# Performance work log

Hardware: AMD Instinct MI355X
Metric: run time of the kernel (lower is better)

Reference implementation:

```python
import jax, jax.numpy as jnp
import numpy as np

N_NODES = 50000
N_EDGES = 600000
EMB_DIM = 128
HIDDEN = 128
BN_EPS = 1e-5


def setup_inputs() -> dict:
    key = jax.random.key(0)
    ks = jax.random.split(key, 8)
    s_in = 1.0 / np.sqrt(EMB_DIM)
    s_h = 1.0 / np.sqrt(HIDDEN)
    return {
        "x_idx": jnp.arange(N_NODES, dtype=jnp.int32),
        "edge_index": jax.random.randint(ks[0], (2, N_EDGES), 0, N_NODES, dtype=jnp.int32),
        "emb_table": jax.random.normal(ks[1], (N_NODES, EMB_DIM), jnp.float32),
        # ClusterGCNConv: lin_out (bias=False) and lin_root (bias=False)
        "W_out": jax.random.uniform(ks[2], (HIDDEN, EMB_DIM), jnp.float32, -s_in, s_in),
        "W_root": jax.random.uniform(ks[3], (HIDDEN, EMB_DIM), jnp.float32, -s_in, s_in),
        "bn0_gamma": jnp.ones((HIDDEN,), jnp.float32),
        "bn0_beta": jnp.zeros((HIDDEN,), jnp.float32),
        # SGConv 1 (K=1, add_self_loops=True, Linear with bias)
        "W_sg1": jax.random.uniform(ks[4], (HIDDEN, HIDDEN), jnp.float32, -s_h, s_h),
        "b_sg1": jnp.zeros((HIDDEN,), jnp.float32),
        "bn1_gamma": jnp.ones((HIDDEN,), jnp.float32),
        "bn1_beta": jnp.zeros((HIDDEN,), jnp.float32),
        # SGConv 2 (final layer)
        "W_sg2": jax.random.uniform(ks[5], (HIDDEN, HIDDEN), jnp.float32, -s_h, s_h),
        "b_sg2": jnp.zeros((HIDDEN,), jnp.float32),
    }


def _cluster_gcn(x, row, col, W_out, W_root, n):
    # PyG ClusterGCNConv (add_self_loops=False, diag_lambda=0, bias=False):
    # out[c] = sum_{(r->c)} (1/deg(c)) * x[r];  return out @ W_out^T + x @ W_root^T
    deg = jax.ops.segment_sum(jnp.ones_like(col, dtype=x.dtype), col, num_segments=n)
    deg_inv = 1.0 / jnp.maximum(deg, 1.0)
    msg = x[row] * deg_inv[col][:, None]                  # [E, D]
    agg = jax.ops.segment_sum(msg, col, num_segments=n)   # [N, D]
    return agg @ W_out.T + x @ W_root.T


def _sg_conv(x, row, col, W, b, n):
    # PyG SGConv K=1 with gcn_norm: A_hat = D^{-1/2}(A+I)D^{-1/2}, then Linear.
    loop = jnp.arange(n, dtype=row.dtype)
    r = jnp.concatenate([row, loop])
    c = jnp.concatenate([col, loop])
    deg = jax.ops.segment_sum(jnp.ones_like(c, dtype=x.dtype), c, num_segments=n)
    dis = jnp.where(deg > 0, jax.lax.rsqrt(jnp.maximum(deg, 1e-12)), 0.0)
    ew = dis[r] * dis[c]                                   # [E+N]
    agg = jax.ops.segment_sum(x[r] * ew[:, None], c, num_segments=n)
    return agg @ W.T + b


def _bn(x, gamma, beta):
    # BatchNorm1d in training mode: batch statistics, biased variance.
    mu = x.mean(axis=0)
    var = ((x - mu) ** 2).mean(axis=0)
    return (x - mu) * jax.lax.rsqrt(var + BN_EPS) * gamma + beta


def reference(x_idx, edge_index, emb_table, W_out, W_root, bn0_gamma, bn0_beta,
              W_sg1, b_sg1, bn1_gamma, bn1_beta, W_sg2, b_sg2):
    n = emb_table.shape[0]
    row, col = edge_index[0], edge_index[1]
    x = emb_table[x_idx]                                   # [N, D]
    # layer 0: ClusterGCNConv -> BN -> ReLU (dropout p=0)
    x = _cluster_gcn(x, row, col, W_out, W_root, n)
    x = jax.nn.relu(_bn(x, bn0_gamma, bn0_beta))
    # layer 1: SGConv -> BN -> ReLU
    x = _sg_conv(x, row, col, W_sg1, b_sg1, n)
    x = jax.nn.relu(_bn(x, bn1_gamma, bn1_beta))
    # final SGConv
    return _sg_conv(x, row, col, W_sg2, b_sg2, n)
```

## Files before the change

kernel.cpp:

```cpp
#include <hip/hip_runtime.h>
#include <stdint.h>

#define NN 50000
#define NE 600000
#define DD 128
#define BN_EPS 1e-5f

typedef __attribute__((ext_vector_type(8))) short short8;
typedef __attribute__((ext_vector_type(4))) float f32x4;

__device__ __forceinline__ float bf2f(uint16_t u) {
    union { uint32_t u; float f; } v; v.u = ((uint32_t)u) << 16; return v.f;
}
__device__ __forceinline__ uint16_t f2bf(float f) {
    union { float f; uint32_t u; } v; v.f = f;
    return (uint16_t)((v.u + 0x7FFFu + ((v.u >> 16) & 1u)) >> 16);
}
__device__ __forceinline__ float lo16(uint32_t v) { return bf2f((uint16_t)(v & 0xFFFFu)); }
__device__ __forceinline__ float hi16(uint32_t v) { return bf2f((uint16_t)(v >> 16)); }

__global__ void k_count(const int* __restrict__ col, int* __restrict__ cnt) {
    int e = blockIdx.x * 256 + threadIdx.x;
    if (e < NE) atomicAdd(&cnt[col[e]], 1);
}

__global__ void k_bsum(const int* __restrict__ cnt, int* __restrict__ bsum) {
    __shared__ int s[256];
    int i = blockIdx.x * 256 + threadIdx.x;
    s[threadIdx.x] = (i < NN) ? cnt[i] : 0;
    __syncthreads();
    for (int d = 128; d > 0; d >>= 1) {
        if (threadIdx.x < d) s[threadIdx.x] += s[threadIdx.x + d];
        __syncthreads();
    }
    if (threadIdx.x == 0) bsum[blockIdx.x] = s[0];
}

__global__ void k_bscan(int* __restrict__ bsum, int nb) {
    __shared__ int s[256];
    int t = threadIdx.x;
    int v = (t < nb) ? bsum[t] : 0;
    s[t] = v;
    __syncthreads();
    for (int d = 1; d < 256; d <<= 1) {
        int add = (t >= d) ? s[t - d] : 0;
        __syncthreads();
        s[t] += add;
        __syncthreads();
    }
    if (t < nb) bsum[t] = s[t] - v;
}

__global__ void k_off(const int* __restrict__ cnt, const int* __restrict__ bsum,
                      int* __restrict__ off, float* __restrict__ deginv,
                      float* __restrict__ dis) {
    __shared__ int s[256];
    int t = threadIdx.x;
    int i = blockIdx.x * 256 + t;
    int v = (i < NN) ? cnt[i] : 0;
    s[t] = v;
    __syncthreads();
    for (int d = 1; d < 256; d <<= 1) {
        int add = (t >= d) ? s[t - d] : 0;
        __syncthreads();
        s[t] += add;
        __syncthreads();
    }
    if (i < NN) {
        int excl = s[t] - v + bsum[blockIdx.x];
        off[i] = excl;
        deginv[i] = 1.0f / fmaxf((float)v, 1.0f);
        dis[i] = rsqrtf((float)v + 1.0f);
        if (i == NN - 1) off[NN] = excl + v;
    }
}

__global__ void k_fill(const int* __restrict__ ei, const int* __restrict__ off,
                       int* __restrict__ fill, int* __restrict__ csr_row) {
    int e = blockIdx.x * 256 + threadIdx.x;
    if (e < NE) {
        int c = ei[NE + e];
        int p = atomicAdd(&fill[c], 1);
        csr_row[off[c] + p] = ei[e];
    }
}

__global__ void k_gather(const int* __restrict__ x_idx, const float* __restrict__ emb,
                         uint16_t* __restrict__ xb) {
    int idx = blockIdx.x * 256 + threadIdx.x;
    if (idx >= NN * 32) return;
    int node = idx >> 5, c4 = (idx & 31) << 2;
    int src = x_idx[node];
    float4 v = *(const float4*)(emb + (size_t)src * DD + c4);
    ushort4 o;
    o.x = f2bf(v.x); o.y = f2bf(v.y); o.z = f2bf(v.z); o.w = f2bf(v.w);
    *(ushort4*)(xb + (size_t)node * DD + c4) = o;
}

template<int MODE>
__global__ __launch_bounds__(256)
void k_agg(const uint16_t* __restrict__ xb, const int* __restrict__ off,
           const int* __restrict__ csr_row, const float* __restrict__ deginv,
           const float* __restrict__ dis, uint16_t* __restrict__ aggb) {
    int node = blockIdx.x * 4 + (threadIdx.x >> 6);
    if (node >= NN) return;
    int lane = threadIdx.x & 63;
    const uint32_t* __restrict__ xw = (const uint32_t*)xb;
    float a0 = 0.0f, a1 = 0.0f;
    if (MODE == 1) {
        uint32_t v = xw[(size_t)node * 64 + lane];
        a0 = lo16(v); a1 = hi16(v);
    }
    int s = off[node], e = off[node + 1];
    for (int base = s; base < e; base += 64) {
        int cnt = min(e - base, 64);
        int idxv = (lane < cnt) ? csr_row[base + lane] : 0;
        int i = 0;
        for (; i + 4 <= cnt; i += 4) {
            int r0 = __builtin_amdgcn_readlane(idxv, i);
            int r1 = __builtin_amdgcn_readlane(idxv, i + 1);
            int r2 = __builtin_amdgcn_readlane(idxv, i + 2);
            int r3 = __builtin_amdgcn_readlane(idxv, i + 3);
            uint32_t v0 = xw[(size_t)r0 * 64 + lane];
            uint32_t v1 = xw[(size_t)r1 * 64 + lane];
            uint32_t v2 = xw[(size_t)r2 * 64 + lane];
            uint32_t v3 = xw[(size_t)r3 * 64 + lane];
            a0 += lo16(v0); a1 += hi16(v0);
            a0 += lo16(v1); a1 += hi16(v1);
            a0 += lo16(v2); a1 += hi16(v2);
            a0 += lo16(v3); a1 += hi16(v3);
        }
        for (; i < cnt; ++i) {
            int r = __builtin_amdgcn_readlane(idxv, i);
            uint32_t v = xw[(size_t)r * 64 + lane];
            a0 += lo16(v); a1 += hi16(v);
        }
    }
    float sc = (MODE == 1) ? dis[node] : deginv[node];
    a0 *= sc; a1 *= sc;
    uint32_t o = (uint32_t)f2bf(a0) | ((uint32_t)f2bf(a1) << 16);
    *(uint32_t*)(aggb + (size_t)node * DD + lane * 2) = o;
}

template<bool DUAL, bool STATS, bool BIAS>
__global__ __launch_bounds__(256, 2)
void k_gemm(const uint16_t* __restrict__ A1, const uint16_t* __restrict__ A2,
            const float* __restrict__ W1, const float* __restrict__ W2,
            const float* __restrict__ bias, float* __restrict__ H,
            float* __restrict__ stats) {
    __shared__ uint16_t Alds[128 * 128];
    __shared__ uint16_t Wlds[128 * 128];
    const int t = threadIdx.x;
    const int lane = t & 63, wid = t >> 6;
    const int wm = (wid >> 1) * 64, wn = (wid & 1) * 64;
    const int m0 = blockIdx.x * 128;
    f32x4 zero = {0.0f, 0.0f, 0.0f, 0.0f};
    f32x4 acc[4][4];
    #pragma unroll
    for (int m = 0; m < 4; ++m)
        #pragma unroll
        for (int n = 0; n < 4; ++n) acc[m][n] = zero;

    const int NP = DUAL ? 2 : 1;
    for (int p = 0; p < NP; ++p) {
        const uint16_t* A = (DUAL && p) ? A2 : A1;
        const float* W = (DUAL && p) ? W2 : W1;
        if (p) __syncthreads();
        #pragma unroll
        for (int it = 0; it < 8; ++it) {
            int idx = it * 256 + t;
            int row = idx >> 4, c16 = idx & 15;
            uint32_t boff = (uint32_t)(row * 256 + ((c16 * 16) ^ ((row & 7) << 4)));
            uint4 v = make_uint4(0u, 0u, 0u, 0u);
            if (m0 + row < NN)
                v = *(const uint4*)(A + (size_t)(m0 + row) * DD + c16 * 8);
            *(uint4*)((char*)Alds + boff) = v;
        }
        #pragma unroll
        for (int it = 0; it < 8; ++it) {
            int idx = it * 256 + t;
            int row = idx >> 4, c8 = idx & 15;
            const float* wp = W + row * DD + c8 * 8;
            float4 v0 = *(const float4*)(wp);
            float4 v1 = *(const float4*)(wp + 4);
            uint4 pk;
            pk.x = (uint32_t)f2bf(v0.x) | ((uint32_t)f2bf(v0.y) << 16);
            pk.y = (uint32_t)f2bf(v0.z) | ((uint32_t)f2bf(v0.w) << 16);
            pk.z = (uint32_t)f2bf(v1.x) | ((uint32_t)f2bf(v1.y) << 16);
            pk.w = (uint32_t)f2bf(v1.z) | ((uint32_t)f2bf(v1.w) << 16);
            uint32_t boff = (uint32_t)(row * 256 + ((c8 * 16) ^ ((row & 7) << 4)));
            *(uint4*)((char*)Wlds + boff) = pk;
        }
        __syncthreads();
        #pragma unroll
        for (int ks = 0; ks < 4; ++ks) {
            short8 a[4], b[4];
            int kb = ks * 64 + ((lane >> 4) << 4);
            #pragma unroll
            for (int m = 0; m < 4; ++m) {
                int row = wm + m * 16 + (lane & 15);
                a[m] = *(const short8*)((const char*)Alds + row * 256 + (kb ^ ((row & 7) << 4)));
            }
            #pragma unroll
            for (int n = 0; n < 4; ++n) {
                int row = wn + n * 16 + (lane & 15);
                b[n] = *(const short8*)((const char*)Wlds + row * 256 + (kb ^ ((row & 7) << 4)));
            }
            #pragma unroll
            for (int m = 0; m < 4; ++m)
                #pragma unroll
                for (int n = 0; n < 4; ++n)
                    acc[m][n] = __builtin_amdgcn_mfma_f32_16x16x32_bf16(a[m], b[n], acc[m][n], 0, 0, 0);
        }
    }
    #pragma unroll
    for (int n = 0; n < 4; ++n) {
        int col = wn + n * 16 + (lane & 15);
        float bb = BIAS ? bias[col] : 0.0f;
        float ssum = 0.0f, ssq = 0.0f;
        #pragma unroll
        for (int m = 0; m < 4; ++m) {
            int rbase = m0 + wm + m * 16 + ((lane >> 4) << 2);
            #pragma unroll
            for (int i = 0; i < 4; ++i) {
                int gr = rbase + i;
                if (gr < NN) {
                    float v = acc[m][n][i] + bb;
                    H[(size_t)gr * DD + col] = v;
                    ssum += v; ssq += v * v;
                }
            }
        }
        if (STATS) {
            ssum += __shfl_xor(ssum, 16, 64);
            ssum += __shfl_xor(ssum, 32, 64);
            ssq  += __shfl_xor(ssq, 16, 64);
            ssq  += __shfl_xor(ssq, 32, 64);
            if (lane < 16) {
                atomicAdd(&stats[col], ssum);
                atomicAdd(&stats[DD + col], ssq);
            }
        }
    }
}

__global__ void k_bnprep(float* __restrict__ st, const float* __restrict__ gamma,
                         const float* __restrict__ beta) {
    int c = threadIdx.x;
    if (c < DD) {
        const float invn = 1.0f / (float)NN;
        float mean = st[c] * invn;
        float var = st[DD + c] * invn - mean * mean;
        float sc = gamma[c] * rsqrtf(var + BN_EPS);
        st[256 + c] = sc;
        st[384 + c] = beta[c] - mean * sc;
    }
}

__global__ void k_bnrelu(const float* __restrict__ H, const float* __restrict__ st,
                         const float* __restrict__ dis, uint16_t* __restrict__ xb) {
    int idx = blockIdx.x * 256 + threadIdx.x;
    if (idx >= NN * 32) return;
    int node = idx >> 5, c4 = (idx & 31) << 2;
    float d = dis[node];
    float4 v = *(const float4*)(H + (size_t)node * DD + c4);
    float r0 = fmaxf(v.x * st[256 + c4 + 0] + st[384 + c4 + 0], 0.0f) * d;
    float r1 = fmaxf(v.y * st[256 + c4 + 1] + st[384 + c4 + 1], 0.0f) * d;
    float r2 = fmaxf(v.z * st[256 + c4 + 2] + st[384 + c4 + 2], 0.0f) * d;
    float r3 = fmaxf(v.w * st[256 + c4 + 3] + st[384 + c4 + 3], 0.0f) * d;
    ushort4 o;
    o.x = f2bf(r0); o.y = f2bf(r1); o.z = f2bf(r2); o.w = f2bf(r3);
    *(ushort4*)(xb + (size_t)node * DD + c4) = o;
}

extern "C" void kernel_launch(void* const* d_in, const int* in_sizes, int n_in,
                              void* d_out, int out_size, void* d_ws, size_t ws_size,
                              hipStream_t stream) {
    const int* x_idx   = (const int*)d_in[0];
    const int* ei      = (const int*)d_in[1];
    const float* emb   = (const float*)d_in[2];
    const float* W_out = (const float*)d_in[3];
    const float* W_root= (const float*)d_in[4];
    const float* g0    = (const float*)d_in[5];
    const float* be0   = (const float*)d_in[6];
    const float* W1    = (const float*)d_in[7];
    const float* b1    = (const float*)d_in[8];
    const float* g1    = (const float*)d_in[9];
    const float* be1   = (const float*)d_in[10];
    const float* W2    = (const float*)d_in[11];
    const float* b2    = (const float*)d_in[12];
    float* out = (float*)d_out;

    char* ws = (char*)d_ws;
    size_t o = 0;
    auto carve = [&](size_t bytes) -> void* {
        void* p = ws + o;
        o = (o + bytes + 255) & ~(size_t)255;
        return p;
    };
    int* cnt      = (int*)carve((size_t)NN * 4);
    int* fillp    = (int*)carve((size_t)NN * 4);
    int* off      = (int*)carve((size_t)(NN + 1) * 4);
    int* bsum     = (int*)carve(256 * 4);
    float* deginv = (float*)carve((size_t)NN * 4);
    float* dis    = (float*)carve((size_t)NN * 4);
    int* csr_row  = (int*)carve((size_t)NE * 4);
    uint16_t* xb  = (uint16_t*)carve((size_t)NN * DD * 2);
    uint16_t* aggb= (uint16_t*)carve((size_t)NN * DD * 2);
    float* st0    = (float*)carve(512 * 4);
    float* st1    = (float*)carve(512 * 4);

    hipMemsetAsync(cnt, 0, (size_t)NN * 4, stream);
    hipMemsetAsync(fillp, 0, (size_t)NN * 4, stream);
    hipMemsetAsync(st0, 0, 256 * 4, stream);
    hipMemsetAsync(st1, 0, 256 * 4, stream);

    const int EB = (NE + 255) / 256;
    const int NB = (NN + 255) / 256;
    const int GB = (NN + 127) / 128;
    const int AB = (NN + 3) / 4;
    const int VB = (NN * 32 + 255) / 256;

    k_count<<<EB, 256, 0, stream>>>(ei + NE, cnt);
    k_bsum<<<NB, 256, 0, stream>>>(cnt, bsum);
    k_bscan<<<1, 256, 0, stream>>>(bsum, NB);
    k_off<<<NB, 256, 0, stream>>>(cnt, bsum, off, deginv, dis);
    k_fill<<<EB, 256, 0, stream>>>(ei, off, fillp, csr_row);
    k_gather<<<VB, 256, 0, stream>>>(x_idx, emb, xb);

    k_agg<0><<<AB, 256, 0, stream>>>(xb, off, csr_row, deginv, dis, aggb);
    k_gemm<true, true, false><<<GB, 256, 0, stream>>>(aggb, xb, W_out, W_root, nullptr, out, st0);
    k_bnprep<<<1, 128, 0, stream>>>(st0, g0, be0);
    k_bnrelu<<<VB, 256, 0, stream>>>(out, st0, dis, xb);

    k_agg<1><<<AB, 256, 0, stream>>>(xb, off, csr_row, deginv, dis, aggb);
    k_gemm<false, true, true><<<GB, 256, 0, stream>>>(aggb, nullptr, W1, nullptr, b1, out, st1);
    k_bnprep<<<1, 128, 0, stream>>>(st1, g1, be1);
    k_bnrelu<<<VB, 256, 0, stream>>>(out, st1, dis, xb);

    k_agg<1><<<AB, 256, 0, stream>>>(xb, off, csr_row, deginv, dis, aggb);
    k_gemm<false, false, true><<<GB, 256, 0, stream>>>(aggb, nullptr, W2, nullptr, b2, out, nullptr);
}
```

Measured before the change: 267.8 us.

## Atomic-cursor padded CSR, bf16 intermediates, fused BN prep, wider gather unroll

Replaces the three-kernel prefix scan with an atomic cursor that hands each node a block of edge slots padded to a multiple of 8, filled with a sentinel zero row. The aggregation loop then always issues 8 independent gathers with no tail loop. The GEMMs for the first two layers store bf16 instead of fp32 to halve intermediate traffic, and BN parameter prep is folded into a vectorized bnrelu kernel. Memsets are merged into one. Padding adds up to 7 extra zero-row loads per node, CSR order becomes nondeterministic, and the bf16 intermediate loses precision before BN.

```diff
diff --git a/kernel.cpp b/kernel.cpp
--- a/kernel.cpp
+++ b/kernel.cpp
@@ -24,84 +24,54 @@
     if (e < NE) atomicAdd(&cnt[col[e]], 1);
 }
 
-__global__ void k_bsum(const int* __restrict__ cnt, int* __restrict__ bsum) {
-    __shared__ int s[256];
+__global__ void k_alloc(const int* __restrict__ cnt, int* __restrict__ cursor,
+                        int* __restrict__ off, int* __restrict__ fillp,
+                        float* __restrict__ deginv, float* __restrict__ dis,
+                        int* __restrict__ csr_row) {
     int i = blockIdx.x * 256 + threadIdx.x;
-    s[threadIdx.x] = (i < NN) ? cnt[i] : 0;
-    __syncthreads();
-    for (int d = 128; d > 0; d >>= 1) {
-        if (threadIdx.x < d) s[threadIdx.x] += s[threadIdx.x + d];
-        __syncthreads();
-    }
-    if (threadIdx.x == 0) bsum[blockIdx.x] = s[0];
-}
-
-__global__ void k_bscan(int* __restrict__ bsum, int nb) {
-    __shared__ int s[256];
-    int t = threadIdx.x;
-    int v = (t < nb) ? bsum[t] : 0;
-    s[t] = v;
-    __syncthreads();
-    for (int d = 1; d < 256; d <<= 1) {
-        int add = (t >= d) ? s[t - d] : 0;
-        __syncthreads();
-        s[t] += add;
-        __syncthreads();
-    }
-    if (t < nb) bsum[t] = s[t] - v;
-}
-
-__global__ void k_off(const int* __restrict__ cnt, const int* __restrict__ bsum,
-                      int* __restrict__ off, float* __restrict__ deginv,
-                      float* __restrict__ dis) {
-    __shared__ int s[256];
-    int t = threadIdx.x;
-    int i = blockIdx.x * 256 + t;
-    int v = (i < NN) ? cnt[i] : 0;
-    s[t] = v;
-    __syncthreads();
-    for (int d = 1; d < 256; d <<= 1) {
-        int add = (t >= d) ? s[t - d] : 0;
-        __syncthreads();
-        s[t] += add;
-        __syncthreads();
-    }
-    if (i < NN) {
-        int excl = s[t] - v + bsum[blockIdx.x];
-        off[i] = excl;
-        deginv[i] = 1.0f / fmaxf((float)v, 1.0f);
-        dis[i] = rsqrtf((float)v + 1.0f);
-        if (i == NN - 1) off[NN] = excl + v;
-    }
-}
-
-__global__ void k_fill(const int* __restrict__ ei, const int* __restrict__ off,
-                       int* __restrict__ fill, int* __restrict__ csr_row) {
+    if (i >= NN) return;
+    int deg = cnt[i];
+    int padded = (deg + 7) & ~7;
+    int base = atomicAdd(cursor, padded);
+    off[i] = base;
+    fillp[i] = base;
+    deginv[i] = 1.0f / fmaxf((float)deg, 1.0f);
+    dis[i] = rsqrtf((float)deg + 1.0f);
+    for (int p = deg; p < padded; ++p) csr_row[base + p] = NN;
+}
+
+__global__ void k_fill(const int* __restrict__ ei, int* __restrict__ fillp,
+                       int* __restrict__ csr_row) {
     int e = blockIdx.x * 256 + threadIdx.x;
     if (e < NE) {
         int c = ei[NE + e];
-        int p = atomicAdd(&fill[c], 1);
-        csr_row[off[c] + p] = ei[e];
+        int p = atomicAdd(&fillp[c], 1);
+        csr_row[p] = ei[e];
     }
 }
 
 __global__ void k_gather(const int* __restrict__ x_idx, const float* __restrict__ emb,
                          uint16_t* __restrict__ xb) {
     int idx = blockIdx.x * 256 + threadIdx.x;
-    if (idx >= NN * 32) return;
+    if (idx >= (NN + 1) * 32) return;
     int node = idx >> 5, c4 = (idx & 31) << 2;
-    int src = x_idx[node];
-    float4 v = *(const float4*)(emb + (size_t)src * DD + c4);
     ushort4 o;
-    o.x = f2bf(v.x); o.y = f2bf(v.y); o.z = f2bf(v.z); o.w = f2bf(v.w);
+    if (node == NN) {
+        o.x = 0; o.y = 0; o.z = 0; o.w = 0;
+    } else {
+        int src = x_idx[node];
+        float4 v = *(const float4*)(emb + (size_t)src * DD + c4);
+        o.x = f2bf(v.x); o.y = f2bf(v.y); o.z = f2bf(v.z); o.w = f2bf(v.w);
+    }
     *(ushort4*)(xb + (size_t)node * DD + c4) = o;
 }
 
 template<int MODE>
 __global__ __launch_bounds__(256)
 void k_agg(const uint16_t* __restrict__ xb, const int* __restrict__ off,
-           const int* __restrict__ csr_row, const float* __restrict__ deginv,
-           const float* __restrict__ dis, uint16_t* __restrict__ aggb) {
+           const int* __restrict__ cnt, const int* __restrict__ csr_row,
+           const float* __restrict__ deginv, const float* __restrict__ dis,
+           uint16_t* __restrict__ aggb) {
     int node = blockIdx.x * 4 + (threadIdx.x >> 6);
     if (node >= NN) return;
     int lane = threadIdx.x & 63;
@@ -111,29 +81,20 @@
         uint32_t v = xw[(size_t)node * 64 + lane];
         a0 = lo16(v); a1 = hi16(v);
     }
-    int s = off[node], e = off[node + 1];
-    for (int base = s; base < e; base += 64) {
-        int cnt = min(e - base, 64);
-        int idxv = (lane < cnt) ? csr_row[base + lane] : 0;
-        int i = 0;
-        for (; i + 4 <= cnt; i += 4) {
-            int r0 = __builtin_amdgcn_readlane(idxv, i);
-            int r1 = __builtin_amdgcn_readlane(idxv, i + 1);
-            int r2 = __builtin_amdgcn_readlane(idxv, i + 2);
-            int r3 = __builtin_amdgcn_readlane(idxv, i + 3);
-            uint32_t v0 = xw[(size_t)r0 * 64 + lane];
-            uint32_t v1 = xw[(size_t)r1 * 64 + lane];
-            uint32_t v2 = xw[(size_t)r2 * 64 + lane];
-            uint32_t v3 = xw[(size_t)r3 * 64 + lane];
-            a0 += lo16(v0); a1 += hi16(v0);
-            a0 += lo16(v1); a1 += hi16(v1);
-            a0 += lo16(v2); a1 += hi16(v2);
-            a0 += lo16(v3); a1 += hi16(v3);
-        }
-        for (; i < cnt; ++i) {
-            int r = __builtin_amdgcn_readlane(idxv, i);
-            uint32_t v = xw[(size_t)r * 64 + lane];
-            a0 += lo16(v); a1 += hi16(v);
+    int s = off[node];
+    int padded = (cnt[node] + 7) & ~7;
+    for (int base = 0; base < padded; base += 64) {
+        int rem = min(padded - base, 64);
+        int idxv = (lane < rem) ? csr_row[s + base + lane] : NN;
+        for (int i = 0; i < rem; i += 8) {
+            uint32_t v[8];
+            #pragma unroll
+            for (int u = 0; u < 8; ++u) {
+                int r = __builtin_amdgcn_readlane(idxv, i + u);
+                v[u] = xw[(size_t)r * 64 + lane];
+            }
+            #pragma unroll
+            for (int u = 0; u < 8; ++u) { a0 += lo16(v[u]); a1 += hi16(v[u]); }
         }
     }
     float sc = (MODE == 1) ? dis[node] : deginv[node];
@@ -142,12 +103,12 @@
     *(uint32_t*)(aggb + (size_t)node * DD + lane * 2) = o;
 }
 
-template<bool DUAL, bool STATS, bool BIAS>
+template<bool DUAL, bool STATS, bool BIAS, bool STORE_BF16>
 __global__ __launch_bounds__(256, 2)
 void k_gemm(const uint16_t* __restrict__ A1, const uint16_t* __restrict__ A2,
             const float* __restrict__ W1, const float* __restrict__ W2,
-            const float* __restrict__ bias, float* __restrict__ H,
-            float* __restrict__ stats) {
+            const float* __restrict__ bias, float* __restrict__ Hf,
+            uint16_t* __restrict__ Hb, float* __restrict__ stats) {
     __shared__ uint16_t Alds[128 * 128];
     __shared__ uint16_t Wlds[128 * 128];
     const int t = threadIdx.x;
@@ -226,7 +187,8 @@
                 int gr = rbase + i;
                 if (gr < NN) {
                     float v = acc[m][n][i] + bb;
-                    H[(size_t)gr * DD + col] = v;
+                    if (STORE_BF16) Hb[(size_t)gr * DD + col] = f2bf(v);
+                    else            Hf[(size_t)gr * DD + col] = v;
                     ssum += v; ssq += v * v;
                 }
             }
@@ -244,33 +206,37 @@
     }
 }
 
-__global__ void k_bnprep(float* __restrict__ st, const float* __restrict__ gamma,
-                         const float* __restrict__ beta) {
-    int c = threadIdx.x;
-    if (c < DD) {
+__global__ __launch_bounds__(256)
+void k_bnrelu(const uint16_t* __restrict__ Hb, const float* __restrict__ st,
+              const float* __restrict__ gamma, const float* __restrict__ beta,
+              const float* __restrict__ dis, uint16_t* __restrict__ xb) {
+    __shared__ float s_sc[128], s_of[128];
+    int t = threadIdx.x;
+    if (t < 128) {
         const float invn = 1.0f / (float)NN;
-        float mean = st[c] * invn;
-        float var = st[DD + c] * invn - mean * mean;
-        float sc = gamma[c] * rsqrtf(var + BN_EPS);
-        st[256 + c] = sc;
-        st[384 + c] = beta[c] - mean * sc;
-    }
-}
-
-__global__ void k_bnrelu(const float* __restrict__ H, const float* __restrict__ st,
-                         const float* __restrict__ dis, uint16_t* __restrict__ xb) {
-    int idx = blockIdx.x * 256 + threadIdx.x;
-    if (idx >= NN * 32) return;
-    int node = idx >> 5, c4 = (idx & 31) << 2;
+        float mean = st[t] * invn;
+        float var = st[DD + t] * invn - mean * mean;
+        float sc = gamma[t] * rsqrtf(var + BN_EPS);
+        s_sc[t] = sc;
+        s_of[t] = beta[t] - mean * sc;
+    }
+    __syncthreads();
+    int idx = blockIdx.x * 256 + t;
+    int node = idx >> 4, c8 = (idx & 15) << 3;
+    if (node >= NN) return;
     float d = dis[node];
-    float4 v = *(const float4*)(H + (size_t)node * DD + c4);
-    float r0 = fmaxf(v.x * st[256 + c4 + 0] + st[384 + c4 + 0], 0.0f) * d;
-    float r1 = fmaxf(v.y * st[256 + c4 + 1] + st[384 + c4 + 1], 0.0f) * d;
-    float r2 = fmaxf(v.z * st[256 + c4 + 2] + st[384 + c4 + 2], 0.0f) * d;
-    float r3 = fmaxf(v.w * st[256 + c4 + 3] + st[384 + c4 + 3], 0.0f) * d;
-    ushort4 o;
-    o.x = f2bf(r0); o.y = f2bf(r1); o.z = f2bf(r2); o.w = f2bf(r3);
-    *(ushort4*)(xb + (size_t)node * DD + c4) = o;
+    uint4 h = *(const uint4*)(Hb + (size_t)node * DD + c8);
+    uint32_t hw[4] = {h.x, h.y, h.z, h.w};
+    uint32_t ow[4];
+    #pragma unroll
+    for (int j = 0; j < 4; ++j) {
+        int c = c8 + j * 2;
+        float v0 = fmaxf(lo16(hw[j]) * s_sc[c]     + s_of[c],     0.0f) * d;
+        float v1 = fmaxf(hi16(hw[j]) * s_sc[c + 1] + s_of[c + 1], 0.0f) * d;
+        ow[j] = (uint32_t)f2bf(v0) | ((uint32_t)f2bf(v1) << 16);
+    }
+    uint4 o = make_uint4(ow[0], ow[1], ow[2], ow[3]);
+    *(uint4*)(xb + (size_t)node * DD + c8) = o;
 }
 
 extern "C" void kernel_launch(void* const* d_in, const int* in_sizes, int n_in,
@@ -299,45 +265,44 @@
         return p;
     };
     int* cnt      = (int*)carve((size_t)NN * 4);
+    int* cursor   = (int*)carve(4);
+    float* st0    = (float*)carve(256 * 4);
+    float* st1    = (float*)carve(256 * 4);
+    size_t zlen = o;
     int* fillp    = (int*)carve((size_t)NN * 4);
-    int* off      = (int*)carve((size_t)(NN + 1) * 4);
-    int* bsum     = (int*)carve(256 * 4);
+    int* off      = (int*)carve((size_t)NN * 4);
     float* deginv = (float*)carve((size_t)NN * 4);
     float* dis    = (float*)carve((size_t)NN * 4);
-    int* csr_row  = (int*)carve((size_t)NE * 4);
-    uint16_t* xb  = (uint16_t*)carve((size_t)NN * DD * 2);
+    int* csr_row  = (int*)carve((size_t)(NE + NN * 8) * 4);
+    uint16_t* xb  = (uint16_t*)carve((size_t)(NN + 1) * DD * 2);
     uint16_t* aggb= (uint16_t*)carve((size_t)NN * DD * 2);
-    float* st0    = (float*)carve(512 * 4);
-    float* st1    = (float*)carve(512 * 4);
-
-    hipMemsetAsync(cnt, 0, (size_t)NN * 4, stream);
-    hipMemsetAsync(fillp, 0, (size_t)NN * 4, stream);
-    hipMemsetAsync(st0, 0, 256 * 4, stream);
-    hipMemsetAsync(st1, 0, 256 * 4, stream);
+    uint16_t* hb  = (uint16_t*)carve((size_t)NN * DD * 2);
+
+    hipMemsetAsync(ws, 0, zlen, stream);
 
     const int EB = (NE + 255) / 256;
     const int NB = (NN + 255) / 256;
     const int GB = (NN + 127) / 128;
     const int AB = (NN + 3) / 4;
-    const int VB = (NN * 32 + 255) / 256;
+    const int VB = ((NN + 1) * 32 + 255) / 256;
+    const int BB = (NN * 16 + 255) / 256;
 
     k_count<<<EB, 256, 0, stream>>>(ei + NE, cnt);
-    k_bsum<<<NB, 256, 0, stream>>>(cnt, bsum);
-    k_bscan<<<1, 256, 0, stream>>>(bsum, NB);
-    k_off<<<NB, 256, 0, stream>>>(cnt, bsum, off, deginv, dis);
-    k_fill<<<EB, 256, 0, stream>>>(ei, off, fillp, csr_row);
+    k_alloc<<<NB, 256, 0, stream>>>(cnt, cursor, off, fillp, deginv, dis, csr_row);
+    k_fill<<<EB, 256, 0, stream>>>(ei, fillp, csr_row);
     k_gather<<<VB, 256, 0, stream>>>(x_idx, emb, xb);
 
-    k_agg<0><<<AB, 256, 0, stream>>>(xb, off, csr_row, deginv, dis, aggb);
-    k_gemm<true, true, false><<<GB, 256, 0, stream>>>(aggb, xb, W_out, W_root, nullptr, out, st0);
-    k_bnprep<<<1, 128, 0, stream>>>(st0, g0, be0);
-    k_bnrelu<<<VB, 256, 0, stream>>>(out, st0, dis, xb);
-
-    k_agg<1><<<AB, 256, 0, stream>>>(xb, off, csr_row, deginv, dis, aggb);
-    k_gemm<false, true, true><<<GB, 256, 0, stream>>>(aggb, nullptr, W1, nullptr, b1, out, st1);
-    k_bnprep<<<1, 128, 0, stream>>>(st1, g1, be1);
-    k_bnrelu<<<VB, 256, 0, stream>>>(out, st1, dis, xb);
-
-    k_agg<1><<<AB, 256, 0, stream>>>(xb, off, csr_row, deginv, dis, aggb);
-    k_gemm<false, false, true><<<GB, 256, 0, stream>>>(aggb, nullptr, W2, nullptr, b2, out, nullptr);
-}
+    k_agg<0><<<AB, 256, 0, stream>>>(xb, off, cnt, csr_row, deginv, dis, aggb);
+    k_gemm<true, true, false, true><<<GB, 256, 0, stream>>>(
+        aggb, xb, W_out, W_root, nullptr, nullptr, hb, st0);
+    k_bnrelu<<<BB, 256, 0, stream>>>(hb, st0, g0, be0, dis, xb);
+
+    k_agg<1><<<AB, 256, 0, stream>>>(xb, off, cnt, csr_row, deginv, dis, aggb);
+    k_gemm<false, true, true, true><<<GB, 256, 0, stream>>>(
+        aggb, nullptr, W1, nullptr, b1, nullptr, hb, st1);
+    k_bnrelu<<<BB, 256, 0, stream>>>(hb, st1, g1, be1, dis, xb);
+
+    k_agg<1><<<AB, 256, 0, stream>>>(xb, off, cnt, csr_row, deginv, dis, aggb);
+    k_gemm<false, false, true, false><<<GB, 256, 0, stream>>>(
+        aggb, nullptr, W2, nullptr, b2, out, nullptr, nullptr);
+}
```

Result: no change. 266.1 us (-0.6%).
